# Kernel optimization log

Hardware: AMD Instinct MI355X
Metric: run time of the kernel (lower is better)

## Reference

```python
import jax, jax.numpy as jnp
import numpy as np

N_FFT = 1024
HOP_LENGTH = 256
N_BANDS = 128


def setup_inputs() -> dict:
    key = jax.random.key(0)
    k1, k2 = jax.random.split(key)
    B, C, T = 16, 1, 1001
    filter_bands = jax.random.uniform(k1, (B, C, N_BANDS, T), dtype=jnp.float32)
    # uniform [0,1); reference applies *2-1 to match torch.rand(...)*2-1
    noise = jax.random.uniform(k2, (B, C, (T - 1) * HOP_LENGTH), dtype=jnp.float32)
    return {"filter_bands": filter_bands, "noise": noise}


def reference(filter_bands, noise):
    B, C, F_bands, T = filter_bands.shape
    pad = N_FFT // 2

    noise = noise * 2.0 - 1.0                      # [-1, 1)
    padded = jnp.pad(noise, ((0, 0), (0, 0), (pad, pad)))  # (B,C,L+N_FFT)

    # unfold: T frames of length N_FFT with stride HOP_LENGTH
    frame_idx = np.arange(T)[:, None] * HOP_LENGTH + np.arange(N_FFT)[None, :]
    frames = padded[:, :, frame_idx]               # (B,C,T,N_FFT)

    # nearest-neighbor interpolation of bands to N_FFT//2 (torch 'nearest': floor(i*in/out))
    band_idx = (np.arange(N_FFT // 2) * F_bands) // (N_FFT // 2)
    filt = jnp.transpose(filter_bands, (0, 1, 3, 2))[:, :, :, band_idx]  # (B,C,T,N_FFT//2)
    dc = jnp.zeros(filt.shape[:-1] + (1,), filt.dtype)
    filt = jnp.concatenate([dc, filt], axis=-1)    # (B,C,T,N_FFT//2+1)

    spec = jnp.fft.rfft(frames)                    # complex64 (B,C,T,513)
    y = jnp.fft.irfft(filt * spec, n=N_FFT)        # (B,C,T,N_FFT)

    # hann window, periodic=False: 0.5*(1 - cos(2*pi*n/(N-1)))
    n = jnp.arange(N_FFT, dtype=y.dtype)
    win = 0.5 * (1.0 - jnp.cos(2.0 * jnp.pi * n / (N_FFT - 1)))
    y = y * win

    # fold = overlap-add
    Lp = padded.shape[-1]
    out = jnp.zeros((B, C, Lp), y.dtype).at[:, :, frame_idx].add(y)
    return out[:, :, pad:-pad]
```

## Files before the change

kernel.cpp:

```cpp
#include <hip/hip_runtime.h>
#include <math.h>

#define NFFT   1024
#define HOP    256
#define NBANDS 128
#define TFRM   1001
#define BB     16
#define NLEN   256000
#define PADL   512
#define NPAIRS 501

#define PX(a) ((a) + ((a) >> 4))

__global__ __launch_bounds__(256) void zero_and_tables(
    float4* __restrict__ out4, int n4, float* __restrict__ ws)
{
    const int tid = blockIdx.x * 256 + threadIdx.x;
    const float4 z = make_float4(0.0f, 0.0f, 0.0f, 0.0f);
    for (int i = tid; i < n4; i += gridDim.x * 256) out4[i] = z;
    if (tid < 256) {
        float s_, c_;
        sincosf(-6.283185307179586f * (float)tid * (1.0f / 1024.0f), &s_, &c_);
        ws[2 * tid]     = c_;
        ws[2 * tid + 1] = s_;
    } else if (tid < 1280) {
        const int k = tid - 256;
        ws[512 + k] = 0.5f * (1.0f - cosf(6.283185307179586f * (float)k * (1.0f / 1023.0f)))
                      * (1.0f / 1024.0f);
    }
}

template<int NS, int SGN>
__device__ __forceinline__ void r4stage2(const float2* __restrict__ x,
                                         float2* __restrict__ y,
                                         const float2* __restrict__ tw, int j) {
    const int m = j & (NS - 1);
    const float2 a0 = x[PX(j)];
    const float2 a1 = x[PX(j + 256)];
    const float2 a2 = x[PX(j + 512)];
    const float2 a3 = x[PX(j + 768)];
    float v1r, v1i, v2r, v2i, v3r, v3i;
    {
        const float2 w = tw[m * (256 / NS)];
        const float wr1 = w.x, wi1 = (SGN < 0) ? w.y : -w.y;
        const float wr2 = wr1 * wr1 - wi1 * wi1, wi2 = 2.0f * wr1 * wi1;
        const float wr3 = wr2 * wr1 - wi2 * wi1, wi3 = wr2 * wi1 + wi2 * wr1;
        v1r = a1.x * wr1 - a1.y * wi1; v1i = a1.x * wi1 + a1.y * wr1;
        v2r = a2.x * wr2 - a2.y * wi2; v2i = a2.x * wi2 + a2.y * wr2;
        v3r = a3.x * wr3 - a3.y * wi3; v3i = a3.x * wi3 + a3.y * wr3;
    }
    const float t0r = a0.x + v2r, t0i = a0.y + v2i;
    const float t1r = a0.x - v2r, t1i = a0.y - v2i;
    const float t2r = v1r + v3r,  t2i = v1i + v3i;
    const float ur  = v1r - v3r,  ui  = v1i - v3i;
    const float t3r = (SGN < 0) ? ui  : -ui;
    const float t3i = (SGN < 0) ? -ur : ur;
    const int d = ((j & ~(NS - 1)) << 2) + m;
    y[PX(d)]          = make_float2(t0r + t2r, t0i + t2i);
    y[PX(d + NS)]     = make_float2(t1r + t3r, t1i + t3i);
    y[PX(d + 2*NS)]   = make_float2(t0r - t2r, t0i - t2i);
    y[PX(d + 3*NS)]   = make_float2(t1r - t3r, t1i - t3i);
}

__global__ __launch_bounds__(256) void fn_kernel(
    const float* __restrict__ fb,
    const float* __restrict__ noise,
    const float* __restrict__ tbl,
    float* __restrict__ out)
{
    __shared__ float2 b0[1087], b1[1087];
    __shared__ float2 tw[256];
    __shared__ float2 gab[128];

    const int tid = threadIdx.x;
    const int hw  = blockIdx.x;
    const int blk = (hw & 7) * 1002 + (hw >> 3);
    const int b   = blk / NPAIRS;
    const int p   = blk - b * NPAIRS;
    const int ta  = 2 * p;
    const bool has_b    = (ta + 1) < TFRM;
    const bool interior = (p >= 1) & (p <= 498);

    tw[tid] = ((const float2*)tbl)[tid & 255];
    if (tid < NBANDS) {
        const size_t off = (size_t)b * (NBANDS * TFRM) + (size_t)tid * TFRM + ta;
        const float ga_ = fb[off];
        const float gb_ = has_b ? fb[off + 1] : 0.0f;
        gab[tid] = make_float2(ga_, gb_);
    }

    const float* nb = noise + (size_t)b * NLEN;
    const int base = ta * HOP - PADL;
    float2 a0, a1, a2, a3;
    if (interior) {
        const int g = base + tid;
        const float v0 = __builtin_fmaf(nb[g],        2.0f, -1.0f);
        const float v1 = __builtin_fmaf(nb[g + 256],  2.0f, -1.0f);
        const float v2 = __builtin_fmaf(nb[g + 512],  2.0f, -1.0f);
        const float v3 = __builtin_fmaf(nb[g + 768],  2.0f, -1.0f);
        const float v4 = __builtin_fmaf(nb[g + 1024], 2.0f, -1.0f);
        a0 = make_float2(v0, v1);
        a1 = make_float2(v1, v2);
        a2 = make_float2(v2, v3);
        a3 = make_float2(v3, v4);
    } else {
        const int g = base + tid;
        #define LD2(gg) make_float2( \
            ((gg) >= 0 && (gg) < NLEN) ? nb[(gg)] * 2.0f - 1.0f : 0.0f, \
            (has_b && (gg) + HOP >= 0 && (gg) + HOP < NLEN) ? nb[(gg) + HOP] * 2.0f - 1.0f : 0.0f)
        a0 = LD2(g); a1 = LD2(g + 256); a2 = LD2(g + 512); a3 = LD2(g + 768);
        #undef LD2
    }
    {
        const float t0r = a0.x + a2.x, t0i = a0.y + a2.y;
        const float t1r = a0.x - a2.x, t1i = a0.y - a2.y;
        const float t2r = a1.x + a3.x, t2i = a1.y + a3.y;
        const float ur  = a1.x - a3.x, ui  = a1.y - a3.y;
        const float t3r = ui, t3i = -ur;
        const int d = 4 * tid;
        b0[PX(d)]     = make_float2(t0r + t2r, t0i + t2i);
        b0[PX(d + 1)] = make_float2(t1r + t3r, t1i + t3i);
        b0[PX(d + 2)] = make_float2(t0r - t2r, t0i - t2i);
        b0[PX(d + 3)] = make_float2(t1r - t3r, t1i - t3i);
    }
    __syncthreads();

    r4stage2<4,   -1>(b0, b1, tw, tid); __syncthreads();
    r4stage2<16,  -1>(b1, b0, tw, tid); __syncthreads();
    r4stage2<64,  -1>(b0, b1, tw, tid); __syncthreads();
    r4stage2<256, -1>(b1, b0, tw, tid); __syncthreads();

    {
        float2 W[4];
        #pragma unroll
        for (int c = 0; c < 4; ++c) {
            const int k = tid + 256 * c;
            const float2 z1 = b0[PX(k)];
            const float2 z2 = b0[PX((NFFT - k) & (NFFT - 1))];
            if (k == 0) {
                W[c] = make_float2(0.0f, 0.0f);
            } else {
                const int jm = (k < NFFT - k) ? k : NFFT - k;
                const float2 g = gab[(jm - 1) >> 2];
                const float Far = 0.5f * (z1.x + z2.x), Fai = 0.5f * (z1.y - z2.y);
                const float Fbr = 0.5f * (z1.y + z2.y), Fbi = 0.5f * (z2.x - z1.x);
                W[c] = make_float2(g.x * Far - g.y * Fbi, g.x * Fai + g.y * Fbr);
            }
        }
        __syncthreads();
        const float t0r = W[0].x + W[2].x, t0i = W[0].y + W[2].y;
        const float t1r = W[0].x - W[2].x, t1i = W[0].y - W[2].y;
        const float t2r = W[1].x + W[3].x, t2i = W[1].y + W[3].y;
        const float ur  = W[1].x - W[3].x, ui  = W[1].y - W[3].y;
        const float t3r = -ui, t3i = ur;
        const int d = 4 * tid;
        b1[PX(d)]     = make_float2(t0r + t2r, t0i + t2i);
        b1[PX(d + 1)] = make_float2(t1r + t3r, t1i + t3i);
        b1[PX(d + 2)] = make_float2(t0r - t2r, t0i - t2i);
        b1[PX(d + 3)] = make_float2(t1r - t3r, t1i - t3i);
    }
    __syncthreads();

    r4stage2<4,  +1>(b1, b0, tw, tid); __syncthreads();
    r4stage2<16, +1>(b0, b1, tw, tid); __syncthreads();
    r4stage2<64, +1>(b1, b0, tw, tid); __syncthreads();

    {
        const float2 c0 = b0[PX(tid)];
        const float2 c1 = b0[PX(tid + 256)];
        const float2 c2 = b0[PX(tid + 512)];
        const float2 c3 = b0[PX(tid + 768)];
        const float2 w = tw[tid];
        const float wr1 = w.x, wi1 = -w.y;
        const float wr2 = wr1 * wr1 - wi1 * wi1, wi2 = 2.0f * wr1 * wi1;
        const float wr3 = wr2 * wr1 - wi2 * wi1, wi3 = wr2 * wi1 + wi2 * wr1;
        const float v1r = c1.x * wr1 - c1.y * wi1, v1i = c1.x * wi1 + c1.y * wr1;
        const float v2r = c2.x * wr2 - c2.y * wi2, v2i = c2.x * wi2 + c2.y * wr2;
        const float v3r = c3.x * wr3 - c3.y * wi3, v3i = c3.x * wi3 + c3.y * wr3;
        const float t0r = c0.x + v2r, t0i = c0.y + v2i;
        const float t1r = c0.x - v2r, t1i = c0.y - v2i;
        const float t2r = v1r + v3r,  t2i = v1i + v3i;
        const float ur  = v1r - v3r,  ui  = v1i - v3i;
        const float t3r = -ui, t3i = ur;
        float2 r[4];
        r[0] = make_float2(t0r + t2r, t0i + t2i);
        r[1] = make_float2(t1r + t3r, t1i + t3i);
        r[2] = make_float2(t0r - t2r, t0i - t2i);
        r[3] = make_float2(t1r - t3r, t1i - t3i);

        const float* win = tbl + 512;
        float wv[4];
        #pragma unroll
        for (int c = 0; c < 4; ++c) wv[c] = win[tid + 256 * c];
        float s[5];
        s[0] = r[0].x * wv[0];
        s[1] = r[1].x * wv[1] + r[0].y * wv[0];
        s[2] = r[2].x * wv[2] + r[1].y * wv[1];
        s[3] = r[3].x * wv[3] + r[2].y * wv[2];
        s[4] =                  r[3].y * wv[3];

        float* ob = out + (size_t)b * NLEN;
        if (interior) {
            #pragma unroll
            for (int c = 0; c < 5; ++c) {
                atomicAdd(&ob[base + tid + 256 * c], s[c]);
            }
        } else {
            #pragma unroll
            for (int c = 0; c < 5; ++c) {
                const int pa = base + tid + 256 * c;
                if (pa >= 0 && pa < NLEN) atomicAdd(&ob[pa], s[c]);
            }
        }
    }
}

extern "C" void kernel_launch(void* const* d_in, const int* in_sizes, int n_in,
                              void* d_out, int out_size, void* d_ws, size_t ws_size,
                              hipStream_t stream) {
    const float* fb    = (const float*)d_in[0];
    const float* noise = (const float*)d_in[1];
    float* out = (float*)d_out;
    float* tbl = (float*)d_ws;

    zero_and_tables<<<2048, 256, 0, stream>>>((float4*)out, out_size / 4, tbl);

    const int grid = BB * NPAIRS;
    fn_kernel<<<grid, 256, 0, stream>>>(fb, noise, tbl, out);
}
```

Measured before the change: 110.5 us.

## Process four frame pairs per block and accumulate overlap-add in registers

Each block now handles four consecutive frame pairs, eight frames in all, and keeps their windowed overlap-add contributions in an 11-element register accumulator. It writes the five fully-owned output segments with plain stores and uses atomics only for the boundary segments shared with neighbouring blocks. This cuts global atomic traffic and block count, and launch bounds now request 8 blocks per CU. In exchange the grid is about four times smaller (2016 blocks) with more serial work per block, and register pressure goes up.

```diff
diff --git a/kernel.cpp b/kernel.cpp
--- a/kernel.cpp
+++ b/kernel.cpp
@@ -9,6 +9,7 @@
 #define NLEN   256000
 #define PADL   512
 #define NPAIRS 501
+#define QPB    126
 
 #define PX(a) ((a) + ((a) >> 4))
 
@@ -62,7 +63,7 @@
     y[PX(d + 3*NS)]   = make_float2(t1r - t3r, t1i - t3i);
 }
 
-__global__ __launch_bounds__(256) void fn_kernel(
+__global__ __launch_bounds__(256, 8) void fn_kernel(
     const float* __restrict__ fb,
     const float* __restrict__ noise,
     const float* __restrict__ tbl,
@@ -74,142 +75,161 @@
 
     const int tid = threadIdx.x;
     const int hw  = blockIdx.x;
-    const int blk = (hw & 7) * 1002 + (hw >> 3);
-    const int b   = blk / NPAIRS;
-    const int p   = blk - b * NPAIRS;
-    const int ta  = 2 * p;
-    const bool has_b    = (ta + 1) < TFRM;
-    const bool interior = (p >= 1) & (p <= 498);
+    const int blk = (hw & 7) * 252 + (hw >> 3);
+    const int b   = blk / QPB;
+    const int q   = blk - b * QPB;
+    const bool blk_interior = (q >= 1) & (q <= 123);
 
     tw[tid] = ((const float2*)tbl)[tid & 255];
-    if (tid < NBANDS) {
-        const size_t off = (size_t)b * (NBANDS * TFRM) + (size_t)tid * TFRM + ta;
-        const float ga_ = fb[off];
-        const float gb_ = has_b ? fb[off + 1] : 0.0f;
-        gab[tid] = make_float2(ga_, gb_);
-    }
-
-    const float* nb = noise + (size_t)b * NLEN;
-    const int base = ta * HOP - PADL;
-    float2 a0, a1, a2, a3;
-    if (interior) {
-        const int g = base + tid;
-        const float v0 = __builtin_fmaf(nb[g],        2.0f, -1.0f);
-        const float v1 = __builtin_fmaf(nb[g + 256],  2.0f, -1.0f);
-        const float v2 = __builtin_fmaf(nb[g + 512],  2.0f, -1.0f);
-        const float v3 = __builtin_fmaf(nb[g + 768],  2.0f, -1.0f);
-        const float v4 = __builtin_fmaf(nb[g + 1024], 2.0f, -1.0f);
-        a0 = make_float2(v0, v1);
-        a1 = make_float2(v1, v2);
-        a2 = make_float2(v2, v3);
-        a3 = make_float2(v3, v4);
+    const float* nb  = noise + (size_t)b * NLEN;
+    const float* win = tbl + 512;
+    const int base_blk = 2048 * q - PADL;
+
+    float wv[4];
+    #pragma unroll
+    for (int c = 0; c < 4; ++c) wv[c] = win[tid + 256 * c];
+
+    float s[11];
+    #pragma unroll
+    for (int i = 0; i < 11; ++i) s[i] = 0.0f;
+
+    #pragma unroll
+    for (int pp = 0; pp < 4; ++pp) {
+        const int p = 4 * q + pp;
+        if (p < NPAIRS) {
+            const int  ta    = 2 * p;
+            const bool has_b = (ta + 1) < TFRM;
+            const bool pint  = (p >= 1) & (p <= 498);
+
+            __syncthreads();
+            if (tid < NBANDS) {
+                const size_t off = (size_t)b * (NBANDS * TFRM) + (size_t)tid * TFRM + ta;
+                const float ga_ = fb[off];
+                const float gb_ = has_b ? fb[off + 1] : 0.0f;
+                gab[tid] = make_float2(ga_, gb_);
+            }
+
+            const int base = ta * HOP - PADL;
+            float2 a0, a1, a2, a3;
+            if (pint) {
+                const int g = base + tid;
+                const float v0 = __builtin_fmaf(nb[g],        2.0f, -1.0f);
+                const float v1 = __builtin_fmaf(nb[g + 256],  2.0f, -1.0f);
+                const float v2 = __builtin_fmaf(nb[g + 512],  2.0f, -1.0f);
+                const float v3 = __builtin_fmaf(nb[g + 768],  2.0f, -1.0f);
+                const float v4 = __builtin_fmaf(nb[g + 1024], 2.0f, -1.0f);
+                a0 = make_float2(v0, v1);
+                a1 = make_float2(v1, v2);
+                a2 = make_float2(v2, v3);
+                a3 = make_float2(v3, v4);
+            } else {
+                const int g = base + tid;
+                #define LD2(gg) make_float2( \
+                    ((gg) >= 0 && (gg) < NLEN) ? nb[(gg)] * 2.0f - 1.0f : 0.0f, \
+                    (has_b && (gg) + HOP >= 0 && (gg) + HOP < NLEN) ? nb[(gg) + HOP] * 2.0f - 1.0f : 0.0f)
+                a0 = LD2(g); a1 = LD2(g + 256); a2 = LD2(g + 512); a3 = LD2(g + 768);
+                #undef LD2
+            }
+            {
+                const float t0r = a0.x + a2.x, t0i = a0.y + a2.y;
+                const float t1r = a0.x - a2.x, t1i = a0.y - a2.y;
+                const float t2r = a1.x + a3.x, t2i = a1.y + a3.y;
+                const float ur  = a1.x - a3.x, ui  = a1.y - a3.y;
+                const float t3r = ui, t3i = -ur;
+                const int d = 4 * tid;
+                b0[PX(d)]     = make_float2(t0r + t2r, t0i + t2i);
+                b0[PX(d + 1)] = make_float2(t1r + t3r, t1i + t3i);
+                b0[PX(d + 2)] = make_float2(t0r - t2r, t0i - t2i);
+                b0[PX(d + 3)] = make_float2(t1r - t3r, t1i - t3i);
+            }
+            __syncthreads();
+
+            r4stage2<4,   -1>(b0, b1, tw, tid); __syncthreads();
+            r4stage2<16,  -1>(b1, b0, tw, tid); __syncthreads();
+            r4stage2<64,  -1>(b0, b1, tw, tid); __syncthreads();
+            r4stage2<256, -1>(b1, b0, tw, tid); __syncthreads();
+
+            {
+                float2 W[4];
+                #pragma unroll
+                for (int c = 0; c < 4; ++c) {
+                    const int k = tid + 256 * c;
+                    const float2 z1 = b0[PX(k)];
+                    const float2 z2 = b0[PX((NFFT - k) & (NFFT - 1))];
+                    if (k == 0) {
+                        W[c] = make_float2(0.0f, 0.0f);
+                    } else {
+                        const int jm = (k < NFFT - k) ? k : NFFT - k;
+                        const float2 g = gab[(jm - 1) >> 2];
+                        const float Far = 0.5f * (z1.x + z2.x), Fai = 0.5f * (z1.y - z2.y);
+                        const float Fbr = 0.5f * (z1.y + z2.y), Fbi = 0.5f * (z2.x - z1.x);
+                        W[c] = make_float2(g.x * Far - g.y * Fbi, g.x * Fai + g.y * Fbr);
+                    }
+                }
+                const float t0r = W[0].x + W[2].x, t0i = W[0].y + W[2].y;
+                const float t1r = W[0].x - W[2].x, t1i = W[0].y - W[2].y;
+                const float t2r = W[1].x + W[3].x, t2i = W[1].y + W[3].y;
+                const float ur  = W[1].x - W[3].x, ui  = W[1].y - W[3].y;
+                const float t3r = -ui, t3i = ur;
+                const int d = 4 * tid;
+                b1[PX(d)]     = make_float2(t0r + t2r, t0i + t2i);
+                b1[PX(d + 1)] = make_float2(t1r + t3r, t1i + t3i);
+                b1[PX(d + 2)] = make_float2(t0r - t2r, t0i - t2i);
+                b1[PX(d + 3)] = make_float2(t1r - t3r, t1i - t3i);
+            }
+            __syncthreads();
+
+            r4stage2<4,  +1>(b1, b0, tw, tid); __syncthreads();
+            r4stage2<16, +1>(b0, b1, tw, tid); __syncthreads();
+            r4stage2<64, +1>(b1, b0, tw, tid); __syncthreads();
+
+            {
+                const float2 c0 = b0[PX(tid)];
+                const float2 c1 = b0[PX(tid + 256)];
+                const float2 c2 = b0[PX(tid + 512)];
+                const float2 c3 = b0[PX(tid + 768)];
+                const float2 w = tw[tid];
+                const float wr1 = w.x, wi1 = -w.y;
+                const float wr2 = wr1 * wr1 - wi1 * wi1, wi2 = 2.0f * wr1 * wi1;
+                const float wr3 = wr2 * wr1 - wi2 * wi1, wi3 = wr2 * wi1 + wi2 * wr1;
+                const float v1r = c1.x * wr1 - c1.y * wi1, v1i = c1.x * wi1 + c1.y * wr1;
+                const float v2r = c2.x * wr2 - c2.y * wi2, v2i = c2.x * wi2 + c2.y * wr2;
+                const float v3r = c3.x * wr3 - c3.y * wi3, v3i = c3.x * wi3 + c3.y * wr3;
+                const float t0r = c0.x + v2r, t0i = c0.y + v2i;
+                const float t1r = c0.x - v2r, t1i = c0.y - v2i;
+                const float t2r = v1r + v3r,  t2i = v1i + v3i;
+                const float ur  = v1r - v3r,  ui  = v1i - v3i;
+                const float t3r = -ui, t3i = ur;
+                float2 r[4];
+                r[0] = make_float2(t0r + t2r, t0i + t2i);
+                r[1] = make_float2(t1r + t3r, t1i + t3i);
+                r[2] = make_float2(t0r - t2r, t0i - t2i);
+                r[3] = make_float2(t1r - t3r, t1i - t3i);
+
+                #pragma unroll
+                for (int c = 0; c < 4; ++c) {
+                    s[2 * pp + c]     += r[c].x * wv[c];
+                    s[2 * pp + 1 + c] += r[c].y * wv[c];
+                }
+            }
+        }
+    }
+
+    float* ob = out + (size_t)b * NLEN;
+    if (blk_interior) {
+        #pragma unroll
+        for (int c = 0; c < 11; ++c) {
+            const int pos = base_blk + tid + 256 * c;
+            if (c >= 3 && c <= 7) ob[pos] = s[c];
+            else atomicAdd(&ob[pos], s[c]);
+        }
     } else {
-        const int g = base + tid;
-        #define LD2(gg) make_float2( \
-            ((gg) >= 0 && (gg) < NLEN) ? nb[(gg)] * 2.0f - 1.0f : 0.0f, \
-            (has_b && (gg) + HOP >= 0 && (gg) + HOP < NLEN) ? nb[(gg) + HOP] * 2.0f - 1.0f : 0.0f)
-        a0 = LD2(g); a1 = LD2(g + 256); a2 = LD2(g + 512); a3 = LD2(g + 768);
-        #undef LD2
-    }
-    {
-        const float t0r = a0.x + a2.x, t0i = a0.y + a2.y;
-        const float t1r = a0.x - a2.x, t1i = a0.y - a2.y;
-        const float t2r = a1.x + a3.x, t2i = a1.y + a3.y;
-        const float ur  = a1.x - a3.x, ui  = a1.y - a3.y;
-        const float t3r = ui, t3i = -ur;
-        const int d = 4 * tid;
-        b0[PX(d)]     = make_float2(t0r + t2r, t0i + t2i);
-        b0[PX(d + 1)] = make_float2(t1r + t3r, t1i + t3i);
-        b0[PX(d + 2)] = make_float2(t0r - t2r, t0i - t2i);
-        b0[PX(d + 3)] = make_float2(t1r - t3r, t1i - t3i);
-    }
-    __syncthreads();
-
-    r4stage2<4,   -1>(b0, b1, tw, tid); __syncthreads();
-    r4stage2<16,  -1>(b1, b0, tw, tid); __syncthreads();
-    r4stage2<64,  -1>(b0, b1, tw, tid); __syncthreads();
-    r4stage2<256, -1>(b1, b0, tw, tid); __syncthreads();
-
-    {
-        float2 W[4];
         #pragma unroll
-        for (int c = 0; c < 4; ++c) {
-            const int k = tid + 256 * c;
-            const float2 z1 = b0[PX(k)];
-            const float2 z2 = b0[PX((NFFT - k) & (NFFT - 1))];
-            if (k == 0) {
-                W[c] = make_float2(0.0f, 0.0f);
-            } else {
-                const int jm = (k < NFFT - k) ? k : NFFT - k;
-                const float2 g = gab[(jm - 1) >> 2];
-                const float Far = 0.5f * (z1.x + z2.x), Fai = 0.5f * (z1.y - z2.y);
-                const float Fbr = 0.5f * (z1.y + z2.y), Fbi = 0.5f * (z2.x - z1.x);
-                W[c] = make_float2(g.x * Far - g.y * Fbi, g.x * Fai + g.y * Fbr);
-            }
-        }
-        __syncthreads();
-        const float t0r = W[0].x + W[2].x, t0i = W[0].y + W[2].y;
-        const float t1r = W[0].x - W[2].x, t1i = W[0].y - W[2].y;
-        const float t2r = W[1].x + W[3].x, t2i = W[1].y + W[3].y;
-        const float ur  = W[1].x - W[3].x, ui  = W[1].y - W[3].y;
-        const float t3r = -ui, t3i = ur;
-        const int d = 4 * tid;
-        b1[PX(d)]     = make_float2(t0r + t2r, t0i + t2i);
-        b1[PX(d + 1)] = make_float2(t1r + t3r, t1i + t3i);
-        b1[PX(d + 2)] = make_float2(t0r - t2r, t0i - t2i);
-        b1[PX(d + 3)] = make_float2(t1r - t3r, t1i - t3i);
-    }
-    __syncthreads();
-
-    r4stage2<4,  +1>(b1, b0, tw, tid); __syncthreads();
-    r4stage2<16, +1>(b0, b1, tw, tid); __syncthreads();
-    r4stage2<64, +1>(b1, b0, tw, tid); __syncthreads();
-
-    {
-        const float2 c0 = b0[PX(tid)];
-        const float2 c1 = b0[PX(tid + 256)];
-        const float2 c2 = b0[PX(tid + 512)];
-        const float2 c3 = b0[PX(tid + 768)];
-        const float2 w = tw[tid];
-        const float wr1 = w.x, wi1 = -w.y;
-        const float wr2 = wr1 * wr1 - wi1 * wi1, wi2 = 2.0f * wr1 * wi1;
-        const float wr3 = wr2 * wr1 - wi2 * wi1, wi3 = wr2 * wi1 + wi2 * wr1;
-        const float v1r = c1.x * wr1 - c1.y * wi1, v1i = c1.x * wi1 + c1.y * wr1;
-        const float v2r = c2.x * wr2 - c2.y * wi2, v2i = c2.x * wi2 + c2.y * wr2;
-        const float v3r = c3.x * wr3 - c3.y * wi3, v3i = c3.x * wi3 + c3.y * wr3;
-        const float t0r = c0.x + v2r, t0i = c0.y + v2i;
-        const float t1r = c0.x - v2r, t1i = c0.y - v2i;
-        const float t2r = v1r + v3r,  t2i = v1i + v3i;
-        const float ur  = v1r - v3r,  ui  = v1i - v3i;
-        const float t3r = -ui, t3i = ur;
-        float2 r[4];
-        r[0] = make_float2(t0r + t2r, t0i + t2i);
-        r[1] = make_float2(t1r + t3r, t1i + t3i);
-        r[2] = make_float2(t0r - t2r, t0i - t2i);
-        r[3] = make_float2(t1r - t3r, t1i - t3i);
-
-        const float* win = tbl + 512;
-        float wv[4];
-        #pragma unroll
-        for (int c = 0; c < 4; ++c) wv[c] = win[tid + 256 * c];
-        float s[5];
-        s[0] = r[0].x * wv[0];
-        s[1] = r[1].x * wv[1] + r[0].y * wv[0];
-        s[2] = r[2].x * wv[2] + r[1].y * wv[1];
-        s[3] = r[3].x * wv[3] + r[2].y * wv[2];
-        s[4] =                  r[3].y * wv[3];
-
-        float* ob = out + (size_t)b * NLEN;
-        if (interior) {
-            #pragma unroll
-            for (int c = 0; c < 5; ++c) {
-                atomicAdd(&ob[base + tid + 256 * c], s[c]);
-            }
-        } else {
-            #pragma unroll
-            for (int c = 0; c < 5; ++c) {
-                const int pa = base + tid + 256 * c;
-                if (pa >= 0 && pa < NLEN) atomicAdd(&ob[pa], s[c]);
+        for (int c = 0; c < 11; ++c) {
+            const int pos = base_blk + tid + 256 * c;
+            if (pos >= 0 && pos < NLEN) {
+                if (c >= 3 && c <= 7) ob[pos] = s[c];
+                else atomicAdd(&ob[pos], s[c]);
             }
         }
     }
@@ -225,6 +245,6 @@
 
     zero_and_tables<<<2048, 256, 0, stream>>>((float4*)out, out_size / 4, tbl);
 
-    const int grid = BB * NPAIRS;
+    const int grid = BB * QPB;
     fn_kernel<<<grid, 256, 0, stream>>>(fb, noise, tbl, out);
 }
```

Result: slower. 122.5 us (+10.8%).
